# Performance work log

Hardware: AMD Instinct MI355X
Metric: run time of the kernel (lower is better)

Reference implementation:

```python
import jax, jax.numpy as jnp
import numpy as np

B, S, M, H, P, T = 32, 400, 400, 200, 16, 4

def setup_inputs() -> dict:
    key = jax.random.key(0)
    ks = jax.random.split(key, 20)
    sc = 0.05
    inp = {
        'att': jax.random.normal(ks[0], (B, S, M), jnp.float32),
        'mod': jax.random.normal(ks[1], (B, S, M), jnp.float32),
        'mask': jnp.ones((B, S), jnp.float32),
        # LSTMCell: input 2*M, hidden H, gate order i,f,g,o
        'lstm_Wih': jax.random.normal(ks[2], (4 * H, 2 * M), jnp.float32) * sc,
        'lstm_Whh': jax.random.normal(ks[3], (4 * H, H), jnp.float32) * sc,
        'lstm_bih': jnp.zeros((4 * H,), jnp.float32),
        'lstm_bhh': jnp.zeros((4 * H,), jnp.float32),
    }
    for pfx, off in (('s', 4), ('e', 11)):
        inp[pfx + '_rW'] = jax.random.normal(ks[off + 0], (H, 2 * M + H), jnp.float32) * sc
        inp[pfx + '_W1'] = jax.random.normal(ks[off + 1], (P * H, M + H), jnp.float32) * sc
        inp[pfx + '_b1'] = jnp.zeros((P * H,), jnp.float32)
        inp[pfx + '_W2'] = jax.random.normal(ks[off + 2], (P * H, H), jnp.float32) * sc
        inp[pfx + '_b2'] = jnp.zeros((P * H,), jnp.float32)
        inp[pfx + '_W3'] = jax.random.normal(ks[off + 3], (P, 2 * H), jnp.float32) * sc
        inp[pfx + '_b3'] = jnp.zeros((P,), jnp.float32)
    return inp

def _gather(mod, idx):
    # mod:[B,S,M], idx:[B] -> [B,M]
    return jnp.take_along_axis(mod, idx[:, None, None], axis=1)[:, 0, :]

def _lstm_cell(x, h, c, Wih, Whh, bih, bhh):
    g = x @ Wih.T + bih + h @ Whh.T + bhh  # [B,4H]
    i, f, gg, o = jnp.split(g, 4, axis=1)
    c2 = jax.nn.sigmoid(f) * c + jax.nn.sigmoid(i) * jnp.tanh(gg)
    h2 = jax.nn.sigmoid(o) * jnp.tanh(c2)
    return h2, c2

def _hmn(mod, h, us, ue, mask, rW, W1, b1, W2, b2, W3, b3):
    r = jnp.tanh(jnp.concatenate([h, us, ue], 1) @ rW.T)  # [B,H]
    x = jnp.concatenate([mod, jnp.broadcast_to(r[:, None, :], (B, S, H))], 2)  # [B,S,M+H]
    m1 = (x @ W1.T + b1).reshape(B, S, P, H).max(2)   # maxout 1
    m2 = (m1 @ W2.T + b2).reshape(B, S, P, H).max(2)  # maxout 2
    logits = (jnp.concatenate([m1, m2], 2) @ W3.T + b3).max(2)  # [B,S]
    logits = jnp.where(mask > 0, logits, -1e30)
    return jax.nn.log_softmax(logits, axis=1)

def reference(att, mod, mask, lstm_Wih, lstm_Whh, lstm_bih, lstm_bhh,
              s_rW, s_W1, s_b1, s_W2, s_b2, s_W3, s_b3,
              e_rW, e_W1, e_b1, e_W2, e_b2, e_W3, e_b3):
    s_prev = jnp.zeros((B,), jnp.int32)
    e_prev = jnp.sum(mask, 1).astype(jnp.int32) - 1
    h = jnp.zeros((B, H), mod.dtype)
    c = jnp.zeros((B, H), mod.dtype)
    log_p1s, log_p2s = [], []
    for _ in range(T):
        u_s = _gather(mod, s_prev)
        u_e = _gather(mod, e_prev)
        h, c = _lstm_cell(jnp.concatenate([u_s, u_e], 1), h, c,
                          lstm_Wih, lstm_Whh, lstm_bih, lstm_bhh)
        lp1 = _hmn(mod, h, u_s, u_e, mask, s_rW, s_W1, s_b1, s_W2, s_b2, s_W3, s_b3)
        s_prev = jnp.argmax(lp1, axis=1).astype(jnp.int32)
        u_s = _gather(mod, s_prev)
        lp2 = _hmn(mod, h, u_s, u_e, mask, e_rW, e_W1, e_b1, e_W2, e_b2, e_W3, e_b3)
        e_prev = jnp.argmax(lp2, axis=1).astype(jnp.int32)
        log_p1s.append(lp1)
        log_p2s.append(lp2)
    return jnp.stack(log_p1s, 1), jnp.stack(log_p2s, 1)  # each [B,T,S]
```

## Files before the change

kernel.cpp:

```cpp
#include <hip/hip_runtime.h>
#include <math.h>

#define NB 32
#define NS 400
#define NM 400
#define NH 200
#define NP 16
#define NT 4
#define NBS (NB*NS)
#define NPH (NP*NH)
#define NX  (2*NM)
#define NG  (4*NH)
#define NR  (2*NM+NH)
#define K1  1280
#define K2  640

typedef __attribute__((ext_vector_type(8))) short short8v;
typedef __attribute__((ext_vector_type(4))) float f32x4;
typedef __attribute__((ext_vector_type(4))) unsigned short us4;
typedef unsigned short ushort;

__device__ __forceinline__ float sigf(float x){ return 1.0f/(1.0f+expf(-x)); }

__device__ __forceinline__ ushort f2bf(float x){
  union{float f; unsigned u;} v; v.f=x;
  unsigned r = v.u + 0x7fffu + ((v.u>>16)&1u);
  return (ushort)(r>>16);
}
__device__ __forceinline__ float bf2f(ushort u){
  union{float f; unsigned v;} x; x.v = ((unsigned)u)<<16; return x.f;
}
__device__ __forceinline__ float wave_sum(float v){
  #pragma unroll
  for (int o=32;o>0;o>>=1) v += __shfl_xor(v, o);
  return v;
}

__global__ __launch_bounds__(256) void init_kernel(const float* __restrict__ mask,
    float* __restrict__ h, float* __restrict__ c,
    int* __restrict__ sprev, int* __restrict__ eprev){
  int b = blockIdx.x, tid = threadIdx.x;
  __shared__ float red[256];
  float s = 0.f;
  for (int i=tid;i<NS;i+=256) s += mask[(size_t)b*NS+i];
  red[tid]=s; __syncthreads();
  for (int st=128;st>0;st>>=1){ if(tid<st) red[tid]+=red[tid+st]; __syncthreads(); }
  if (tid==0){ sprev[b]=0; eprev[b]=(int)red[0]-1; }
  for (int i=tid;i<NH;i+=256){ h[(size_t)b*NH+i]=0.f; c[(size_t)b*NH+i]=0.f; }
}

__global__ __launch_bounds__(256) void conv_mod_k(const float* __restrict__ in, ushort* __restrict__ out){
  for (size_t i = (size_t)blockIdx.x*256+threadIdx.x; i < (size_t)NBS*NM; i += (size_t)gridDim.x*256){
    int r = (int)(i/NM), k = (int)(i%NM);
    float x = in[i];
    ushort h = f2bf(x); ushort lo = f2bf(x - bf2f(h));
    ushort* o = out + (size_t)r*K1;
    o[k]=h; o[NM+k]=lo; o[2*NM+k]=h;
  }
}
__global__ __launch_bounds__(256) void conv_w1_k(const float* __restrict__ in, ushort* __restrict__ out){
  for (size_t i = (size_t)blockIdx.x*256+threadIdx.x; i < (size_t)NPH*NM; i += (size_t)gridDim.x*256){
    int j = (int)(i/NM), k = (int)(i%NM);
    int jp = (j%NH)*NP + j/NH;
    float x = in[(size_t)j*(NM+NH)+k];
    ushort h = f2bf(x); ushort lo = f2bf(x - bf2f(h));
    ushort* o = out + (size_t)jp*K1;
    o[k]=h; o[NM+k]=h; o[2*NM+k]=lo;
  }
}
__global__ __launch_bounds__(256) void conv_w2_k(const float* __restrict__ in, ushort* __restrict__ out){
  for (size_t i = (size_t)blockIdx.x*256+threadIdx.x; i < (size_t)NPH*NH; i += (size_t)gridDim.x*256){
    int j = (int)(i/NH), k = (int)(i%NH);
    int jp = (j%NH)*NP + j/NH;
    float x = in[(size_t)j*NH+k];
    ushort h = f2bf(x); ushort lo = f2bf(x - bf2f(h));
    ushort* o = out + (size_t)jp*K2;
    o[k]=h; o[NH+k]=h; o[2*NH+k]=lo;
  }
}
__global__ __launch_bounds__(256) void conv_w1r_k(const float* __restrict__ in, float* __restrict__ out){
  for (size_t i = (size_t)blockIdx.x*256+threadIdx.x; i < (size_t)NH*NPH; i += (size_t)gridDim.x*256){
    int k = (int)(i/NPH), jp = (int)(i%NPH);
    int hh = jp>>4, p = jp&15, j = p*NH + hh;
    out[i] = in[(size_t)j*(NM+NH) + NM + k];
  }
}
__global__ __launch_bounds__(256) void permv_k(const float* __restrict__ in, float* __restrict__ out){
  int i = blockIdx.x*256+threadIdx.x;
  if (i < NPH) out[(i%NH)*NP + i/NH] = in[i];
}
__global__ __launch_bounds__(256) void pad_zero_k(ushort* __restrict__ p, int stride, int start, int width, int rows){
  for (size_t i = (size_t)blockIdx.x*256+threadIdx.x; i < (size_t)rows*width; i += (size_t)gridDim.x*256){
    int r = (int)(i/width), j = (int)(i%width);
    p[(size_t)r*stride + start + j] = 0;
  }
}

__global__ __launch_bounds__(256) void lstm_gates(const float* __restrict__ mod,
    const int* __restrict__ sprev, const int* __restrict__ eprev,
    const float* __restrict__ h,
    const float* __restrict__ Wih, const float* __restrict__ Whh,
    const float* __restrict__ bih, const float* __restrict__ bhh,
    float* __restrict__ gs){
  int b=blockIdx.x, tid=threadIdx.x;
  __shared__ float xs[NX+NH];
  const float* us = mod + ((size_t)b*NS + sprev[b])*NM;
  const float* ue = mod + ((size_t)b*NS + eprev[b])*NM;
  for (int i=tid;i<NM;i+=256){ xs[i]=us[i]; xs[NM+i]=ue[i]; }
  for (int i=tid;i<NH;i+=256) xs[NX+i]=h[(size_t)b*NH+i];
  __syncthreads();
  int w=tid>>6, lane=tid&63;
  int j = blockIdx.y*4 + w;
  const float* wih = Wih + (size_t)j*NX;
  const float* whh = Whh + (size_t)j*NH;
  float acc=0.f;
  for (int k=lane;k<NX;k+=64) acc += xs[k]*wih[k];
  for (int k=lane;k<NH;k+=64) acc += xs[NX+k]*whh[k];
  acc = wave_sum(acc);
  if (lane==0) gs[(size_t)b*NG+j] = acc + bih[j] + bhh[j];
}
__global__ __launch_bounds__(256) void lstm_update(const float* __restrict__ gs,
    float* __restrict__ h, float* __restrict__ c){
  int b=blockIdx.x, j=threadIdx.x;
  if (j<NH){
    float iv=gs[(size_t)b*NG+j], fv=gs[(size_t)b*NG+NH+j];
    float gv=gs[(size_t)b*NG+2*NH+j], ov=gs[(size_t)b*NG+3*NH+j];
    float c2 = sigf(fv)*c[(size_t)b*NH+j] + sigf(iv)*tanhf(gv);
    c[(size_t)b*NH+j]=c2;
    h[(size_t)b*NH+j]=sigf(ov)*tanhf(c2);
  }
}

__global__ __launch_bounds__(256) void r_kernel(const float* __restrict__ mod,
    const int* __restrict__ sprev, const int* __restrict__ eprev,
    const float* __restrict__ h, const float* __restrict__ rW,
    float* __restrict__ rbuf){
  int b=blockIdx.x, tid=threadIdx.x;
  __shared__ float zs[NR];
  const float* us = mod + ((size_t)b*NS + sprev[b])*NM;
  const float* ue = mod + ((size_t)b*NS + eprev[b])*NM;
  for (int i=tid;i<NH;i+=256) zs[i]=h[(size_t)b*NH+i];
  for (int i=tid;i<NM;i+=256){ zs[NH+i]=us[i]; zs[NH+NM+i]=ue[i]; }
  __syncthreads();
  int w=tid>>6, lane=tid&63;
  int j = blockIdx.y*4 + w;
  const float* wr = rW + (size_t)j*NR;
  float acc=0.f;
  for (int k=lane;k<NR;k+=64) acc += zs[k]*wr[k];
  acc = wave_sum(acc);
  if (lane==0) rbuf[(size_t)b*NH+j] = tanhf(acc);
}

__global__ __launch_bounds__(256) void prer_kernel(const float* __restrict__ rbuf,
    const float* __restrict__ W1rT, const float* __restrict__ b1p,
    float* __restrict__ prer){
  int b=blockIdx.x, tid=threadIdx.x;
  __shared__ float rs[NH];
  if (tid < NH) rs[tid] = rbuf[(size_t)b*NH+tid];
  __syncthreads();
  int jp = blockIdx.y*256 + tid;
  if (jp < NPH){
    float acc = b1p[jp];
    #pragma unroll 8
    for (int k=0;k<NH;k++) acc += rs[k]*W1rT[(size_t)k*NPH + jp];
    prer[(size_t)b*NPH + jp] = acc;
  }
}

template<int MODE>
__global__ __launch_bounds__(256) void gemm_fused(
    const ushort* __restrict__ A, const ushort* __restrict__ W, int ldk,
    const float* __restrict__ bias, void* __restrict__ outp){
  __shared__ __align__(16) ushort As[2][128*32];
  __shared__ __align__(16) ushort Bs[2][128*32];
  __shared__ float biasLds[2][128];
  __shared__ float outT[128][8];
  const int tid = threadIdx.x;
  const int i0 = blockIdx.x*128, j0 = blockIdx.y*128;
  const int b0 = i0/NS;
  if (MODE==0){
    if (tid<128) biasLds[0][tid] = bias[(size_t)b0*NPH + j0 + tid];
    else { int b1r = (i0+127)/NS; biasLds[1][tid-128] = bias[(size_t)b1r*NPH + j0 + (tid-128)]; }
  } else {
    if (tid<128) biasLds[0][tid] = bias[j0+tid];
  }
  const int l = tid&63, w = tid>>6;
  const int wr = w>>1, wc = w&1;
  const int srow = tid>>2, slot = tid&3;
  const int fr = l&15, fk = l>>4;
  const int ksteps = ldk>>5;
  auto stage = [&](int buf, int kt){
    #pragma unroll
    for (int r=0;r<2;r++){
      int row = r*64 + srow;
      int ss  = slot ^ ((row>>1)&3);
      const ushort* ga = A + (size_t)(i0+row)*ldk + kt*32 + ss*8;
      const ushort* gb = W + (size_t)(j0+row)*ldk + kt*32 + ss*8;
      __builtin_amdgcn_global_load_lds((const __attribute__((address_space(1))) void*)ga,
          (__attribute__((address_space(3))) void*)(&As[buf][row*32 + slot*8]), 16, 0, 0);
      __builtin_amdgcn_global_load_lds((const __attribute__((address_space(1))) void*)gb,
          (__attribute__((address_space(3))) void*)(&Bs[buf][row*32 + slot*8]), 16, 0, 0);
    }
  };
  f32x4 acc[4][4] = {};
  stage(0, 0);
  __syncthreads();
  int cur = 0;
  for (int kt=0; kt<ksteps; kt++){
    if (kt+1 < ksteps) stage(cur^1, kt+1);
    short8v af[4], bf[4];
    #pragma unroll
    for (int m=0;m<4;m++){
      int row = wr*64 + m*16 + fr;
      int sl = fk ^ ((row>>1)&3);
      af[m] = *(const short8v*)(&As[cur][row*32 + sl*8]);
    }
    #pragma unroll
    for (int n=0;n<4;n++){
      int row = wc*64 + n*16 + fr;
      int sl = fk ^ ((row>>1)&3);
      bf[n] = *(const short8v*)(&Bs[cur][row*32 + sl*8]);
    }
    #pragma unroll
    for (int m=0;m<4;m++)
      #pragma unroll
      for (int n=0;n<4;n++)
        acc[m][n] = __builtin_amdgcn_mfma_f32_16x16x32_bf16(af[m], bf[n], acc[m][n], 0,0,0);
    __syncthreads();
    cur ^= 1;
  }
  const int blim = (b0+1)*NS;
  #pragma unroll
  for (int m=0;m<4;m++){
    #pragma unroll
    for (int n=0;n<4;n++){
      int colL = wc*64 + n*16 + fr;
      int rbase = wr*64 + m*16 + fk*4;
      #pragma unroll
      for (int reg=0; reg<4; reg++){
        int rowL = rbase + reg;
        float bv;
        if (MODE==0) bv = ((i0+rowL) >= blim) ? biasLds[1][colL] : biasLds[0][colL];
        else bv = biasLds[0][colL];
        float v = acc[m][n][reg] + bv;
        v = fmaxf(v, __shfl_xor(v,1));
        v = fmaxf(v, __shfl_xor(v,2));
        v = fmaxf(v, __shfl_xor(v,4));
        v = fmaxf(v, __shfl_xor(v,8));
        if (fr==0) outT[rowL][wc*4+n] = v;
      }
    }
  }
  __syncthreads();
  {
    int rowL = tid>>1;
    int c4 = (tid&1)*4;
    int absrow = i0 + rowL;
    int hg0 = (j0>>4) + c4;
    float v0=outT[rowL][c4], v1=outT[rowL][c4+1], v2=outT[rowL][c4+2], v3=outT[rowL][c4+3];
    if (MODE==0){
      ushort* o = (ushort*)outp + (size_t)absrow*K2 + hg0;
      ushort h0=f2bf(v0), h1=f2bf(v1), h2=f2bf(v2), h3=f2bf(v3);
      ushort l0=f2bf(v0-bf2f(h0)), l1=f2bf(v1-bf2f(h1)), l2=f2bf(v2-bf2f(h2)), l3=f2bf(v3-bf2f(h3));
      *(us4*)(o)        = (us4){h0,h1,h2,h3};
      *(us4*)(o+NH)     = (us4){l0,l1,l2,l3};
      *(us4*)(o+2*NH)   = (us4){h0,h1,h2,h3};
    } else {
      float* o = (float*)outp + (size_t)absrow*NH + hg0;
      *(f32x4*)o = (f32x4){v0,v1,v2,v3};
    }
  }
}

__global__ __launch_bounds__(256) void logits_main(const ushort* __restrict__ m1e,
    const float* __restrict__ m2, const float* __restrict__ W3, const float* __restrict__ b3,
    const float* __restrict__ mask, float* __restrict__ lg){
  int b=blockIdx.x;
  int s=blockIdx.y*256+threadIdx.x;
  if (s >= NS) return;
  const ushort* a = m1e + (size_t)(b*NS+s)*K2;
  const float4* d = (const float4*)(m2 + (size_t)(b*NS+s)*NH);
  float acc[NP];
  #pragma unroll
  for (int p=0;p<NP;p++) acc[p]=b3[p];
  for (int k=0;k<NH/4;k++){
    us4 hv = *(const us4*)(a + 4*k);
    us4 lv = *(const us4*)(a + NH + 4*k);
    float4 dv = d[k];
    float a0=bf2f(hv.x)+bf2f(lv.x), a1=bf2f(hv.y)+bf2f(lv.y);
    float a2=bf2f(hv.z)+bf2f(lv.z), a3=bf2f(hv.w)+bf2f(lv.w);
    #pragma unroll
    for (int p=0;p<NP;p++){
      const float* wp = W3 + p*(2*NH) + 4*k;
      acc[p] += a0*wp[0]+a1*wp[1]+a2*wp[2]+a3*wp[3];
      const float* w2 = wp + NH;
      acc[p] += dv.x*w2[0]+dv.y*w2[1]+dv.z*w2[2]+dv.w*w2[3];
    }
  }
  float best=acc[0];
  #pragma unroll
  for (int p=1;p<NP;p++) best=fmaxf(best,acc[p]);
  lg[(size_t)b*NS+s] = (mask[(size_t)b*NS+s] > 0.f) ? best : -1e30f;
}

__global__ __launch_bounds__(256) void logits_fin(const float* __restrict__ lg,
    float* __restrict__ out, int t, int* __restrict__ prevIdx){
  int b=blockIdx.x, tid=threadIdx.x;
  __shared__ float rv[256]; __shared__ int ri[256]; __shared__ float sv[256];
  float bv=-INFINITY; int bi=NS;
  for (int s=tid;s<NS;s+=256){ float v=lg[(size_t)b*NS+s]; if (v>bv){bv=v;bi=s;} }
  rv[tid]=bv; ri[tid]=bi; __syncthreads();
  for (int st=128;st>0;st>>=1){
    if (tid<st){
      float v2=rv[tid+st]; int i2=ri[tid+st];
      if (v2>rv[tid] || (v2==rv[tid] && i2<ri[tid])){ rv[tid]=v2; ri[tid]=i2; }
    }
    __syncthreads();
  }
  float mx = rv[0];
  float ps=0.f;
  for (int s=tid;s<NS;s+=256) ps += expf(lg[(size_t)b*NS+s]-mx);
  sv[tid]=ps; __syncthreads();
  for (int st=128;st>0;st>>=1){ if (tid<st) sv[tid]+=sv[tid+st]; __syncthreads(); }
  float lse = mx + logf(sv[0]);
  for (int s=tid;s<NS;s+=256) out[((size_t)b*NT + t)*NS + s] = lg[(size_t)b*NS+s]-lse;
  if (tid==0) prevIdx[b]=ri[0];
}

extern "C" void kernel_launch(void* const* d_in, const int* in_sizes, int n_in,
                              void* d_out, int out_size, void* d_ws, size_t ws_size,
                              hipStream_t stream){
  const float* mod  = (const float*)d_in[1];
  const float* mask = (const float*)d_in[2];
  const float* Wih  = (const float*)d_in[3];
  const float* Whh  = (const float*)d_in[4];
  const float* bih  = (const float*)d_in[5];
  const float* bhh  = (const float*)d_in[6];
  const float* rW[2] = {(const float*)d_in[7],  (const float*)d_in[14]};
  const float* W1[2] = {(const float*)d_in[8],  (const float*)d_in[15]};
  const float* b1[2] = {(const float*)d_in[9],  (const float*)d_in[16]};
  const float* W2[2] = {(const float*)d_in[10], (const float*)d_in[17]};
  const float* b2[2] = {(const float*)d_in[11], (const float*)d_in[18]};
  const float* W3[2] = {(const float*)d_in[12], (const float*)d_in[19]};
  const float* b3[2] = {(const float*)d_in[13], (const float*)d_in[20]};
  float* out[2];
  out[0] = (float*)d_out;
  out[1] = out[0] + (size_t)NB*NT*NS;

  float* wsf = (float*)d_ws;
  size_t off = 0;
  auto carve = [&](size_t n)->size_t{ size_t o=off; off += (n + 63) & ~(size_t)63; return o; };
  float* hbuf   = wsf + carve((size_t)NB*NH);
  float* cbuf   = wsf + carve((size_t)NB*NH);
  float* prer   = wsf + carve((size_t)NB*NPH);
  int*   sprev  = (int*)(wsf + carve(128));
  int*   eprev  = sprev + 32;
  float* m2f    = wsf + carve((size_t)NBS*NH);
  float* b2p[2] = {wsf + carve(NPH), wsf + carve(NPH)};
  float* b1p[2] = {wsf + carve(NPH), wsf + carve(NPH)};
  float* rbuf   = wsf + carve((size_t)NB*NH);
  float* gsbuf  = wsf + carve((size_t)NB*NG);
  float* lgbuf  = wsf + carve((size_t)NB*NS);
  float* W1rT[2]= {wsf + carve((size_t)NH*NPH), wsf + carve((size_t)NH*NPH)};
  ushort* modExp   = (ushort*)(wsf + carve((size_t)NBS*K1/2));
  ushort* W1exp[2] = {(ushort*)(wsf + carve((size_t)NPH*K1/2)),
                      (ushort*)(wsf + carve((size_t)NPH*K1/2))};
  ushort* W2exp[2] = {(ushort*)(wsf + carve((size_t)NPH*K2/2)),
                      (ushort*)(wsf + carve((size_t)NPH*K2/2))};
  ushort* m1exp    = (ushort*)(wsf + carve((size_t)NBS*K2/2));

  init_kernel<<<NB, 256, 0, stream>>>(mask, hbuf, cbuf, sprev, eprev);
  conv_mod_k<<<2048, 256, 0, stream>>>(mod, modExp);
  pad_zero_k<<<256, 256, 0, stream>>>(modExp, K1, 3*NM, K1-3*NM, NBS);
  pad_zero_k<<<256, 256, 0, stream>>>(m1exp, K2, 3*NH, K2-3*NH, NBS);
  for (int net=0; net<2; net++){
    conv_w1_k<<<2048, 256, 0, stream>>>(W1[net], W1exp[net]);
    pad_zero_k<<<64, 256, 0, stream>>>(W1exp[net], K1, 3*NM, K1-3*NM, NPH);
    conv_w2_k<<<1024, 256, 0, stream>>>(W2[net], W2exp[net]);
    pad_zero_k<<<64, 256, 0, stream>>>(W2exp[net], K2, 3*NH, K2-3*NH, NPH);
    conv_w1r_k<<<1024, 256, 0, stream>>>(W1[net], W1rT[net]);
    permv_k<<<(NPH+255)/256, 256, 0, stream>>>(b2[net], b2p[net]);
    permv_k<<<(NPH+255)/256, 256, 0, stream>>>(b1[net], b1p[net]);
  }

  dim3 ggrid(NBS/128, NPH/128);
  for (int t=0; t<NT; t++){
    lstm_gates<<<dim3(NB, NG/4), 256, 0, stream>>>(mod, sprev, eprev, hbuf,
                                                   Wih, Whh, bih, bhh, gsbuf);
    lstm_update<<<NB, 256, 0, stream>>>(gsbuf, hbuf, cbuf);
    for (int net=0; net<2; net++){
      r_kernel<<<dim3(NB, NH/4), 256, 0, stream>>>(mod, sprev, eprev, hbuf, rW[net], rbuf);
      prer_kernel<<<dim3(NB, (NPH+255)/256), 256, 0, stream>>>(rbuf, W1rT[net], b1p[net], prer);
      gemm_fused<0><<<ggrid, 256, 0, stream>>>(modExp, W1exp[net], K1, prer, (void*)m1exp);
      gemm_fused<1><<<ggrid, 256, 0, stream>>>(m1exp, W2exp[net], K2, b2p[net], (void*)m2f);
      logits_main<<<dim3(NB, 2), 256, 0, stream>>>(m1exp, m2f, W3[net], b3[net], mask, lgbuf);
      logits_fin<<<NB, 256, 0, stream>>>(lgbuf, out[net], t, net==0 ? sprev : eprev);
    }
  }
}
```

Baseline: 3.124 ms.

## Triple-buffer GEMM k-loop, fuse small per-step kernels, coalesce conversion writes

```diff
diff --git a/kernel.cpp b/kernel.cpp
--- a/kernel.cpp
+++ b/kernel.cpp
@@ -50,32 +50,41 @@
 }
 
 __global__ __launch_bounds__(256) void conv_mod_k(const float* __restrict__ in, ushort* __restrict__ out){
-  for (size_t i = (size_t)blockIdx.x*256+threadIdx.x; i < (size_t)NBS*NM; i += (size_t)gridDim.x*256){
-    int r = (int)(i/NM), k = (int)(i%NM);
-    float x = in[i];
-    ushort h = f2bf(x); ushort lo = f2bf(x - bf2f(h));
-    ushort* o = out + (size_t)r*K1;
-    o[k]=h; o[NM+k]=lo; o[2*NM+k]=h;
+  for (size_t i = (size_t)blockIdx.x*256+threadIdx.x; i < (size_t)NBS*K1; i += (size_t)gridDim.x*256){
+    int r = (int)(i/K1), k = (int)(i%K1);
+    ushort v = 0;
+    if (k < 3*NM){
+      float x = in[(size_t)r*NM + (k % NM)];
+      ushort h = f2bf(x);
+      v = (k < NM || k >= 2*NM) ? h : f2bf(x - bf2f(h));
+    }
+    out[i] = v;
   }
 }
 __global__ __launch_bounds__(256) void conv_w1_k(const float* __restrict__ in, ushort* __restrict__ out){
-  for (size_t i = (size_t)blockIdx.x*256+threadIdx.x; i < (size_t)NPH*NM; i += (size_t)gridDim.x*256){
-    int j = (int)(i/NM), k = (int)(i%NM);
-    int jp = (j%NH)*NP + j/NH;
-    float x = in[(size_t)j*(NM+NH)+k];
-    ushort h = f2bf(x); ushort lo = f2bf(x - bf2f(h));
-    ushort* o = out + (size_t)jp*K1;
-    o[k]=h; o[NM+k]=h; o[2*NM+k]=lo;
+  for (size_t i = (size_t)blockIdx.x*256+threadIdx.x; i < (size_t)NPH*K1; i += (size_t)gridDim.x*256){
+    int jp = (int)(i/K1), k = (int)(i%K1);
+    int j = (jp&15)*NH + (jp>>4);
+    ushort v = 0;
+    if (k < 3*NM){
+      float x = in[(size_t)j*(NM+NH) + (k % NM)];
+      ushort h = f2bf(x);
+      v = (k < 2*NM) ? h : f2bf(x - bf2f(h));
+    }
+    out[i] = v;
   }
 }
 __global__ __launch_bounds__(256) void conv_w2_k(const float* __restrict__ in, ushort* __restrict__ out){
-  for (size_t i = (size_t)blockIdx.x*256+threadIdx.x; i < (size_t)NPH*NH; i += (size_t)gridDim.x*256){
-    int j = (int)(i/NH), k = (int)(i%NH);
-    int jp = (j%NH)*NP + j/NH;
-    float x = in[(size_t)j*NH+k];
-    ushort h = f2bf(x); ushort lo = f2bf(x - bf2f(h));
-    ushort* o = out + (size_t)jp*K2;
-    o[k]=h; o[NH+k]=h; o[2*NH+k]=lo;
+  for (size_t i = (size_t)blockIdx.x*256+threadIdx.x; i < (size_t)NPH*K2; i += (size_t)gridDim.x*256){
+    int jp = (int)(i/K2), k = (int)(i%K2);
+    int j = (jp&15)*NH + (jp>>4);
+    ushort v = 0;
+    if (k < 3*NH){
+      float x = in[(size_t)j*NH + (k % NH)];
+      ushort h = f2bf(x);
+      v = (k < 2*NH) ? h : f2bf(x - bf2f(h));
+    }
+    out[i] = v;
   }
 }
 __global__ __launch_bounds__(256) void conv_w1r_k(const float* __restrict__ in, float* __restrict__ out){
@@ -119,50 +128,45 @@
   acc = wave_sum(acc);
   if (lane==0) gs[(size_t)b*NG+j] = acc + bih[j] + bhh[j];
 }
-__global__ __launch_bounds__(256) void lstm_update(const float* __restrict__ gs,
-    float* __restrict__ h, float* __restrict__ c){
-  int b=blockIdx.x, j=threadIdx.x;
-  if (j<NH){
-    float iv=gs[(size_t)b*NG+j], fv=gs[(size_t)b*NG+NH+j];
-    float gv=gs[(size_t)b*NG+2*NH+j], ov=gs[(size_t)b*NG+3*NH+j];
-    float c2 = sigf(fv)*c[(size_t)b*NH+j] + sigf(iv)*tanhf(gv);
-    c[(size_t)b*NH+j]=c2;
-    h[(size_t)b*NH+j]=sigf(ov)*tanhf(c2);
-  }
-}
-
-__global__ __launch_bounds__(256) void r_kernel(const float* __restrict__ mod,
+
+__global__ __launch_bounds__(512) void rprer_kernel(const float* __restrict__ mod,
     const int* __restrict__ sprev, const int* __restrict__ eprev,
-    const float* __restrict__ h, const float* __restrict__ rW,
-    float* __restrict__ rbuf){
+    const float* __restrict__ gsb, float* __restrict__ h, float* __restrict__ c,
+    const float* __restrict__ rW, const float* __restrict__ W1rT,
+    const float* __restrict__ b1p, float* __restrict__ prer, int doUpdate){
   int b=blockIdx.x, tid=threadIdx.x;
   __shared__ float zs[NR];
+  __shared__ float rsh[NH];
+  if (doUpdate){
+    if (tid < NH){
+      float iv=gsb[(size_t)b*NG+tid], fv=gsb[(size_t)b*NG+NH+tid];
+      float gv=gsb[(size_t)b*NG+2*NH+tid], ov=gsb[(size_t)b*NG+3*NH+tid];
+      float c2 = sigf(fv)*c[(size_t)b*NH+tid] + sigf(iv)*tanhf(gv);
+      float h2 = sigf(ov)*tanhf(c2);
+      c[(size_t)b*NH+tid]=c2; h[(size_t)b*NH+tid]=h2;
+      zs[tid]=h2;
+    }
+  } else {
+    if (tid < NH) zs[tid] = h[(size_t)b*NH+tid];
+  }
   const float* us = mod + ((size_t)b*NS + sprev[b])*NM;
   const float* ue = mod + ((size_t)b*NS + eprev[b])*NM;
-  for (int i=tid;i<NH;i+=256) zs[i]=h[(size_t)b*NH+i];
-  for (int i=tid;i<NM;i+=256){ zs[NH+i]=us[i]; zs[NH+NM+i]=ue[i]; }
+  for (int i=tid;i<NM;i+=512){ zs[NH+i]=us[i]; zs[NH+NM+i]=ue[i]; }
   __syncthreads();
   int w=tid>>6, lane=tid&63;
-  int j = blockIdx.y*4 + w;
-  const float* wr = rW + (size_t)j*NR;
-  float acc=0.f;
-  for (int k=lane;k<NR;k+=64) acc += zs[k]*wr[k];
-  acc = wave_sum(acc);
-  if (lane==0) rbuf[(size_t)b*NH+j] = tanhf(acc);
-}
-
-__global__ __launch_bounds__(256) void prer_kernel(const float* __restrict__ rbuf,
-    const float* __restrict__ W1rT, const float* __restrict__ b1p,
-    float* __restrict__ prer){
-  int b=blockIdx.x, tid=threadIdx.x;
-  __shared__ float rs[NH];
-  if (tid < NH) rs[tid] = rbuf[(size_t)b*NH+tid];
-  __syncthreads();
-  int jp = blockIdx.y*256 + tid;
-  if (jp < NPH){
+  for (int jj=0; jj<25; jj++){
+    int j = w*25 + jj;
+    const float* wr = rW + (size_t)j*NR;
+    float acc=0.f;
+    for (int k=lane;k<NR;k+=64) acc += zs[k]*wr[k];
+    acc = wave_sum(acc);
+    if (lane==0) rsh[j] = tanhf(acc);
+  }
+  __syncthreads();
+  for (int jp=tid; jp<NPH; jp+=512){
     float acc = b1p[jp];
     #pragma unroll 8
-    for (int k=0;k<NH;k++) acc += rs[k]*W1rT[(size_t)k*NPH + jp];
+    for (int k=0;k<NH;k++) acc += rsh[k]*W1rT[(size_t)k*NPH + jp];
     prer[(size_t)b*NPH + jp] = acc;
   }
 }
@@ -171,8 +175,8 @@
 __global__ __launch_bounds__(256) void gemm_fused(
     const ushort* __restrict__ A, const ushort* __restrict__ W, int ldk,
     const float* __restrict__ bias, void* __restrict__ outp){
-  __shared__ __align__(16) ushort As[2][128*32];
-  __shared__ __align__(16) ushort Bs[2][128*32];
+  __shared__ __align__(16) ushort As[3][128*32];
+  __shared__ __align__(16) ushort Bs[3][128*32];
   __shared__ float biasLds[2][128];
   __shared__ float outT[128][8];
   const int tid = threadIdx.x;
@@ -189,25 +193,32 @@
   const int srow = tid>>2, slot = tid&3;
   const int fr = l&15, fk = l>>4;
   const int ksteps = ldk>>5;
+  const int ss0 = slot ^ ((srow>>1)&3);
+  const int ss1 = slot ^ (((srow+64)>>1)&3);
+  const ushort* gA0 = A + (size_t)(i0+srow)*ldk     + ss0*8;
+  const ushort* gA1 = A + (size_t)(i0+srow+64)*ldk  + ss1*8;
+  const ushort* gB0 = W + (size_t)(j0+srow)*ldk     + ss0*8;
+  const ushort* gB1 = W + (size_t)(j0+srow+64)*ldk  + ss1*8;
+  const int ldsOff = srow*32 + slot*8;
   auto stage = [&](int buf, int kt){
-    #pragma unroll
-    for (int r=0;r<2;r++){
-      int row = r*64 + srow;
-      int ss  = slot ^ ((row>>1)&3);
-      const ushort* ga = A + (size_t)(i0+row)*ldk + kt*32 + ss*8;
-      const ushort* gb = W + (size_t)(j0+row)*ldk + kt*32 + ss*8;
-      __builtin_amdgcn_global_load_lds((const __attribute__((address_space(1))) void*)ga,
-          (__attribute__((address_space(3))) void*)(&As[buf][row*32 + slot*8]), 16, 0, 0);
-      __builtin_amdgcn_global_load_lds((const __attribute__((address_space(1))) void*)gb,
-          (__attribute__((address_space(3))) void*)(&Bs[buf][row*32 + slot*8]), 16, 0, 0);
-    }
+    __builtin_amdgcn_global_load_lds((const __attribute__((address_space(1))) void*)(gA0 + kt*32),
+        (__attribute__((address_space(3))) void*)(&As[buf][ldsOff]), 16, 0, 0);
+    __builtin_amdgcn_global_load_lds((const __attribute__((address_space(1))) void*)(gB0 + kt*32),
+        (__attribute__((address_space(3))) void*)(&Bs[buf][ldsOff]), 16, 0, 0);
+    __builtin_amdgcn_global_load_lds((const __attribute__((address_space(1))) void*)(gA1 + kt*32),
+        (__attribute__((address_space(3))) void*)(&As[buf][64*32 + ldsOff]), 16, 0, 0);
+    __builtin_amdgcn_global_load_lds((const __attribute__((address_space(1))) void*)(gB1 + kt*32),
+        (__attribute__((address_space(3))) void*)(&Bs[buf][64*32 + ldsOff]), 16, 0, 0);
   };
   f32x4 acc[4][4] = {};
   stage(0, 0);
-  __syncthreads();
-  int cur = 0;
+  if (ksteps > 1) stage(1, 1);
+  __syncthreads();
   for (int kt=0; kt<ksteps; kt++){
-    if (kt+1 < ksteps) stage(cur^1, kt+1);
+    if (kt+1 < ksteps) asm volatile("s_waitcnt vmcnt(4)" ::: "memory");
+    else               asm volatile("s_waitcnt vmcnt(0)" ::: "memory");
+    __builtin_amdgcn_s_barrier();
+    const int cur = kt % 3;
     short8v af[4], bf[4];
     #pragma unroll
     for (int m=0;m<4;m++){
@@ -221,14 +232,16 @@
       int sl = fk ^ ((row>>1)&3);
       bf[n] = *(const short8v*)(&Bs[cur][row*32 + sl*8]);
     }
+    asm volatile("s_waitcnt lgkmcnt(0)" ::: "memory");
+    __builtin_amdgcn_sched_barrier(0);
+    if (kt+2 < ksteps) stage((kt+2)%3, kt+2);
     #pragma unroll
     for (int m=0;m<4;m++)
       #pragma unroll
       for (int n=0;n<4;n++)
         acc[m][n] = __builtin_amdgcn_mfma_f32_16x16x32_bf16(af[m], bf[n], acc[m][n], 0,0,0);
-    __syncthreads();
-    cur ^= 1;
-  }
+  }
+  __syncthreads();
   const int blim = (b0+1)*NS;
   #pragma unroll
   for (int m=0;m<4;m++){
@@ -272,45 +285,43 @@
   }
 }
 
-__global__ __launch_bounds__(256) void logits_main(const ushort* __restrict__ m1e,
+__global__ __launch_bounds__(512) void logits_kernel(const ushort* __restrict__ m1e,
     const float* __restrict__ m2, const float* __restrict__ W3, const float* __restrict__ b3,
-    const float* __restrict__ mask, float* __restrict__ lg){
-  int b=blockIdx.x;
-  int s=blockIdx.y*256+threadIdx.x;
-  if (s >= NS) return;
-  const ushort* a = m1e + (size_t)(b*NS+s)*K2;
-  const float4* d = (const float4*)(m2 + (size_t)(b*NS+s)*NH);
-  float acc[NP];
-  #pragma unroll
-  for (int p=0;p<NP;p++) acc[p]=b3[p];
-  for (int k=0;k<NH/4;k++){
-    us4 hv = *(const us4*)(a + 4*k);
-    us4 lv = *(const us4*)(a + NH + 4*k);
-    float4 dv = d[k];
-    float a0=bf2f(hv.x)+bf2f(lv.x), a1=bf2f(hv.y)+bf2f(lv.y);
-    float a2=bf2f(hv.z)+bf2f(lv.z), a3=bf2f(hv.w)+bf2f(lv.w);
-    #pragma unroll
-    for (int p=0;p<NP;p++){
-      const float* wp = W3 + p*(2*NH) + 4*k;
-      acc[p] += a0*wp[0]+a1*wp[1]+a2*wp[2]+a3*wp[3];
-      const float* w2 = wp + NH;
-      acc[p] += dv.x*w2[0]+dv.y*w2[1]+dv.z*w2[2]+dv.w*w2[3];
-    }
-  }
-  float best=acc[0];
-  #pragma unroll
-  for (int p=1;p<NP;p++) best=fmaxf(best,acc[p]);
-  lg[(size_t)b*NS+s] = (mask[(size_t)b*NS+s] > 0.f) ? best : -1e30f;
-}
-
-__global__ __launch_bounds__(256) void logits_fin(const float* __restrict__ lg,
-    float* __restrict__ out, int t, int* __restrict__ prevIdx){
+    const float* __restrict__ mask, float* __restrict__ out, int t, int* __restrict__ prevIdx){
   int b=blockIdx.x, tid=threadIdx.x;
-  __shared__ float rv[256]; __shared__ int ri[256]; __shared__ float sv[256];
+  __shared__ float lg[NS];
+  if (tid < NS){
+    int s = tid;
+    const ushort* a = m1e + (size_t)(b*NS+s)*K2;
+    const float4* d = (const float4*)(m2 + (size_t)(b*NS+s)*NH);
+    float acc[NP];
+    #pragma unroll
+    for (int p=0;p<NP;p++) acc[p]=b3[p];
+    for (int k=0;k<NH/4;k++){
+      us4 hv = *(const us4*)(a + 4*k);
+      us4 lv = *(const us4*)(a + NH + 4*k);
+      float4 dv = d[k];
+      float a0=bf2f(hv.x)+bf2f(lv.x), a1=bf2f(hv.y)+bf2f(lv.y);
+      float a2=bf2f(hv.z)+bf2f(lv.z), a3=bf2f(hv.w)+bf2f(lv.w);
+      #pragma unroll
+      for (int p=0;p<NP;p++){
+        const float* wp = W3 + p*(2*NH) + 4*k;
+        acc[p] += a0*wp[0]+a1*wp[1]+a2*wp[2]+a3*wp[3];
+        const float* w2 = wp + NH;
+        acc[p] += dv.x*w2[0]+dv.y*w2[1]+dv.z*w2[2]+dv.w*w2[3];
+      }
+    }
+    float best=acc[0];
+    #pragma unroll
+    for (int p=1;p<NP;p++) best=fmaxf(best,acc[p]);
+    lg[s] = (mask[(size_t)b*NS+s] > 0.f) ? best : -1e30f;
+  }
+  __syncthreads();
+  __shared__ float rv[512]; __shared__ int ri[512]; __shared__ float sv[512];
   float bv=-INFINITY; int bi=NS;
-  for (int s=tid;s<NS;s+=256){ float v=lg[(size_t)b*NS+s]; if (v>bv){bv=v;bi=s;} }
+  if (tid < NS){ bv = lg[tid]; bi = tid; }
   rv[tid]=bv; ri[tid]=bi; __syncthreads();
-  for (int st=128;st>0;st>>=1){
+  for (int st=256;st>0;st>>=1){
     if (tid<st){
       float v2=rv[tid+st]; int i2=ri[tid+st];
       if (v2>rv[tid] || (v2==rv[tid] && i2<ri[tid])){ rv[tid]=v2; ri[tid]=i2; }
@@ -318,12 +329,11 @@
     __syncthreads();
   }
   float mx = rv[0];
-  float ps=0.f;
-  for (int s=tid;s<NS;s+=256) ps += expf(lg[(size_t)b*NS+s]-mx);
+  float ps = (tid<NS) ? expf(lg[tid]-mx) : 0.f;
   sv[tid]=ps; __syncthreads();
-  for (int st=128;st>0;st>>=1){ if (tid<st) sv[tid]+=sv[tid+st]; __syncthreads(); }
+  for (int st=256;st>0;st>>=1){ if (tid<st) sv[tid]+=sv[tid+st]; __syncthreads(); }
   float lse = mx + logf(sv[0]);
-  for (int s=tid;s<NS;s+=256) out[((size_t)b*NT + t)*NS + s] = lg[(size_t)b*NS+s]-lse;
+  if (tid < NS) out[((size_t)b*NT + t)*NS + tid] = lg[tid]-lse;
   if (tid==0) prevIdx[b]=ri[0];
 }
 
@@ -358,9 +368,7 @@
   float* m2f    = wsf + carve((size_t)NBS*NH);
   float* b2p[2] = {wsf + carve(NPH), wsf + carve(NPH)};
   float* b1p[2] = {wsf + carve(NPH), wsf + carve(NPH)};
-  float* rbuf   = wsf + carve((size_t)NB*NH);
   float* gsbuf  = wsf + carve((size_t)NB*NG);
-  float* lgbuf  = wsf + carve((size_t)NB*NS);
   float* W1rT[2]= {wsf + carve((size_t)NH*NPH), wsf + carve((size_t)NH*NPH)};
   ushort* modExp   = (ushort*)(wsf + carve((size_t)NBS*K1/2));
   ushort* W1exp[2] = {(ushort*)(wsf + carve((size_t)NPH*K1/2)),
@@ -371,13 +379,10 @@
 
   init_kernel<<<NB, 256, 0, stream>>>(mask, hbuf, cbuf, sprev, eprev);
   conv_mod_k<<<2048, 256, 0, stream>>>(mod, modExp);
-  pad_zero_k<<<256, 256, 0, stream>>>(modExp, K1, 3*NM, K1-3*NM, NBS);
   pad_zero_k<<<256, 256, 0, stream>>>(m1exp, K2, 3*NH, K2-3*NH, NBS);
   for (int net=0; net<2; net++){
     conv_w1_k<<<2048, 256, 0, stream>>>(W1[net], W1exp[net]);
-    pad_zero_k<<<64, 256, 0, stream>>>(W1exp[net], K1, 3*NM, K1-3*NM, NPH);
     conv_w2_k<<<1024, 256, 0, stream>>>(W2[net], W2exp[net]);
-    pad_zero_k<<<64, 256, 0, stream>>>(W2exp[net], K2, 3*NH, K2-3*NH, NPH);
     conv_w1r_k<<<1024, 256, 0, stream>>>(W1[net], W1rT[net]);
     permv_k<<<(NPH+255)/256, 256, 0, stream>>>(b2[net], b2p[net]);
     permv_k<<<(NPH+255)/256, 256, 0, stream>>>(b1[net], b1p[net]);
@@ -387,14 +392,13 @@
   for (int t=0; t<NT; t++){
     lstm_gates<<<dim3(NB, NG/4), 256, 0, stream>>>(mod, sprev, eprev, hbuf,
                                                    Wih, Whh, bih, bhh, gsbuf);
-    lstm_update<<<NB, 256, 0, stream>>>(gsbuf, hbuf, cbuf);
     for (int net=0; net<2; net++){
-      r_kernel<<<dim3(NB, NH/4), 256, 0, stream>>>(mod, sprev, eprev, hbuf, rW[net], rbuf);
-      prer_kernel<<<dim3(NB, (NPH+255)/256), 256, 0, stream>>>(rbuf, W1rT[net], b1p[net], prer);
+      rprer_kernel<<<NB, 512, 0, stream>>>(mod, sprev, eprev, gsbuf, hbuf, cbuf,
+                                           rW[net], W1rT[net], b1p[net], prer, net==0);
       gemm_fused<0><<<ggrid, 256, 0, stream>>>(modExp, W1exp[net], K1, prer, (void*)m1exp);
       gemm_fused<1><<<ggrid, 256, 0, stream>>>(m1exp, W2exp[net], K2, b2p[net], (void*)m2f);
-      logits_main<<<dim3(NB, 2), 256, 0, stream>>>(m1exp, m2f, W3[net], b3[net], mask, lgbuf);
-      logits_fin<<<NB, 256, 0, stream>>>(lgbuf, out[net], t, net==0 ? sprev : eprev);
-    }
-  }
-}
+      logits_kernel<<<NB, 512, 0, stream>>>(m1exp, m2f, W3[net], b3[net], mask,
+                                            out[net], t, net==0 ? sprev : eprev);
+    }
+  }
+}
```

After: 4.584 ms. 1.47x slower.
